# Kernel tuning notes

Hardware: AMD Instinct MI355X
Metric: run time of the kernel (lower is better)

The kernel has to match this reference:

```python
import jax, jax.numpy as jnp
import numpy as np

B, S, NGB, NG, DIM = 64, 4096, 13, 48, 3
NCH = [8, 8, 1]
NSHELLS = 8


def setup_inputs() -> dict:
    key = jax.random.key(0)
    ks = jax.random.split(key, 16)
    rng = np.random.default_rng(0)
    # valid row-wise permutations of the N_ngb neighbor slots per group op
    GnnPerms = jnp.asarray(np.argsort(rng.random((NG, NGB)), axis=1), dtype=jnp.int64)
    NNSites = jax.random.randint(ks[0], (NGB, S), 0, S, dtype=jnp.int64)
    SitesToShells = jax.random.randint(ks[1], (S,), 0, NSHELLS, dtype=jnp.int64)
    # block-diagonal (Ng*dim, Ng*dim) cartesian rotation blocks
    blk = rng.normal(size=(NG, DIM, DIM)).astype(np.float32) * 0.5
    gd = np.zeros((NG * DIM, NG * DIM), np.float32)
    for g in range(NG):
        gd[g * DIM:(g + 1) * DIM, g * DIM:(g + 1) * DIM] = blk[g]
    gdiags = jnp.asarray(gd)
    std = 0.2
    return {
        "InStates": jax.random.normal(ks[2], (B, 1, S), jnp.float32),
        "Psi0": jax.random.normal(ks[3], (NCH[0], 1, NGB), jnp.float32) * std,
        "bias0": jax.random.normal(ks[4], (NCH[0], 1), jnp.float32) * std,
        "Psi1": jax.random.normal(ks[5], (NCH[1], NCH[0], NGB), jnp.float32) * std,
        "bias1": jax.random.normal(ks[6], (NCH[1], 1), jnp.float32) * std,
        "Psi2": jax.random.normal(ks[7], (NCH[2], NCH[1], NGB), jnp.float32) * std,
        "bias2": jax.random.normal(ks[8], (NCH[2], 1), jnp.float32) * std,
        "wtVC": jax.random.normal(ks[9], (DIM, NGB), jnp.float32) * std,
        "ShellWeights": jax.random.normal(ks[10], (NSHELLS,), jnp.float32) * std,
        "gdiags": gdiags,
        "GnnPerms": GnnPerms,
        "NNSites": NNSites,
        "SitesToShells": SitesToShells,
    }


def _rearrange(x, NNSites):
    # x: (B, Nch, S) -> (B, Nch*N_ngb, S); subchannel j of channel c holds x[b, c, NNSites[j, s]]
    b, c, s = x.shape
    return x[:, :, NNSites].reshape(b, c * NGB, s)


def _gconv(x, W, b):
    # x: (B, NchIn*N_ngb, S); W: (NchOut, NchIn, N_ngb); b: (NchOut, 1)
    # group-rotated weights: GW[o, g, c*N_ngb+j] = W[o, c, GnnPerms[g, j]]
    GW = _gconv.GW_cache  # set per-call below via closure-free pattern; replaced in reference
    raise NotImplementedError


def reference(InStates, Psi0, bias0, Psi1, bias1, Psi2, bias2, wtVC,
              ShellWeights, gdiags, GnnPerms, NNSites, SitesToShells):
    act = jax.nn.softplus

    def gconv(x, W, b):
        # rotated weights: (NchOut, Ng, NchIn*N_ngb)
        GW = W[:, :, GnnPerms].transpose(0, 2, 1, 3).reshape(W.shape[0], NG, -1)
        h = jnp.einsum('ogk,bks->bogs', GW, x) + b[:, :, None]  # (B, NchOut, Ng, S)
        return act(h).mean(axis=2)                               # group-orbit average

    out = _rearrange(InStates, NNSites)
    for W, b in ((Psi0, bias0), (Psi1, bias1), (Psi2, bias2)):
        out = gconv(out, W, b)                 # (B, NchOut, S)
        out = _rearrange(out, NNSites)         # (B, NchOut*N_ngb, S)
    # vector channel: row g*dim+d of P is wtVC[d, GnnPerms[g]]
    P = wtVC[:, GnnPerms].transpose(1, 0, 2).reshape(NG * DIM, NGB)
    Wvc = gdiags @ P                           # (Ng*dim, N_ngb)
    v = jnp.einsum('kn,bns->bks', Wvc, out)    # (B, Ng*dim, S)
    v = v.reshape(-1, NG, DIM, out.shape[-1]).mean(axis=1)  # (B, dim, S)
    v = v * ShellWeights[SitesToShells]        # per-site shell weighting
    return v.sum(axis=2) / out.shape[-1]       # (B, dim)
```

## Files before the change

### kernel.cpp

```cpp
#include <hip/hip_runtime.h>
#include <hip/hip_bf16.h>

#define BATCH 64
#define SITES 4096
#define NGB 13
#define NGRP 48
#define SDIM 3

#define LOG2E 1.44269504f
#define SPSCALE 0.014440236f

typedef __bf16 bf16x8 __attribute__((ext_vector_type(8)));
typedef float  f32x4  __attribute__((ext_vector_type(4)));

#define OFF_AVC  0
#define OFF_U    64
#define OFF_A0   67648
#define OFF_SW   67648
#define OFF_A1   2164800
#define OFF_PART 4261952
#define UW0H 0
#define UW0L 12288
#define UW1H 24576
#define UW1L 73728
#define UW2H 122880
#define UW2L 129024

__global__ __launch_bounds__(256) void precompute_kernel(
    const float* __restrict__ Psi0, const float* __restrict__ Psi1,
    const float* __restrict__ Psi2, const float* __restrict__ wtVC,
    const float* __restrict__ gdiags, const int* __restrict__ perms,
    float* __restrict__ ws)
{
    float*  Avc = ws + OFF_AVC;
    __bf16* U   = (__bf16*)(ws + OFF_U);
    int t = blockIdx.x * 256 + threadIdx.x;
    if (t < 12288) {
        int k = t & 31, row = t >> 5;
        int o = row / NGRP, g = row - o * NGRP;
        float w = (k < NGB) ? Psi0[o * NGB + perms[g * NGB + k]] * LOG2E : 0.f;
        __bf16 hi = (__bf16)w;
        U[UW0H + t] = hi;
        U[UW0L + t] = (__bf16)(w - (float)hi);
    } else if (t < 61440) {
        int u = t - 12288;
        int k = u & 127, row = u >> 7;
        int o = row / NGRP, g = row - o * NGRP;
        float w = 0.f;
        if (k < 104) { int j = k >> 3, c = k & 7;
                       w = Psi1[(o * 8 + c) * NGB + perms[g * NGB + j]] * LOG2E; }
        __bf16 hi = (__bf16)w;
        U[UW1H + u] = hi;
        U[UW1L + u] = (__bf16)(w - (float)hi);
    } else if (t < 67584) {
        int u = t - 61440;
        int k = u & 127, g = u >> 7;
        float w = 0.f;
        if (k < 104) { int j = k >> 3, c = k & 7;
                       w = Psi2[c * NGB + perms[g * NGB + j]] * LOG2E; }
        __bf16 hi = (__bf16)w;
        U[UW2H + u] = hi;
        U[UW2L + u] = (__bf16)(w - (float)hi);
    } else if (t < 67584 + 39 * NGRP) {
        int t2 = t - 67584;
        int g = t2 % NGRP, u = t2 / NGRP;
        int d = u / NGB, n = u % NGB;
        const int row = g * SDIM + d;
        float s = 0.f;
        for (int k = 0; k < NGRP * SDIM; k++) {
            int g2 = k / SDIM, d2 = k - g2 * SDIM;
            float p = wtVC[d2 * NGB + perms[g2 * NGB + n]];
            s = fmaf(gdiags[row * (NGRP * SDIM) + k], p, s);
        }
        atomicAdd(&Avc[u], s * (1.f / 48.f));
    }
}

__global__ __launch_bounds__(256) void build_sw(
    const float* __restrict__ Avc, const int* __restrict__ NN,
    const int* __restrict__ s2sh, const float* __restrict__ shellw,
    float* __restrict__ SW)
{
    int e = blockIdx.x * 256 + threadIdx.x;
    if (e < NGB * SITES) {
        int n = e / SITES, s = e - n * SITES;
        float wgt = shellw[s2sh[s]] * (SPSCALE / (float)SITES);
        int t = NN[e];
        atomicAdd(&SW[t],             Avc[n] * wgt);
        atomicAdd(&SW[SITES + t],     Avc[NGB + n] * wgt);
        atomicAdd(&SW[2 * SITES + t], Avc[2 * NGB + n] * wgt);
    }
}

template<int NCIN, int NCTOT, int CT, int KPAD, int KEXT, int KSTR,
         int NWAVES, int NWN, int CHUNKS, int FUSED>
__global__ __launch_bounds__(NWAVES * 64) void layer_mfma(
    const float* __restrict__ prev,
    const __bf16* __restrict__ Wh,
    const __bf16* __restrict__ Wl,
    const float* __restrict__ bias,
    const int*   __restrict__ NN,
    const float* __restrict__ SWp,
    float* __restrict__ partial,
    float* __restrict__ out)
{
    constexpr int NTHR   = NWAVES * 64;
    constexpr int M      = NCTOT * NGRP;
    constexpr int MTILES = M / 16, NTILES = CT / 16;
    constexpr int NWM    = NWAVES / NWN;
    constexpr int MT_W   = MTILES / NWM, NT_W = NTILES / NWN;
    constexpr int KT     = KPAD / 32;
    constexpr int GS     = NGB * CT;
    constexpr int SPT    = (GS + NTHR - 1) / NTHR;
    constexpr int CPB    = SITES / CT;
    constexpr int BUF    = CT * KSTR;
    constexpr int BPB    = CPB / CHUNKS;

    static_assert(MT_W * 16 == NGRP, "wave covers exactly one o");
    static_assert(NWM * MT_W == MTILES && NWN * NT_W == NTILES, "");
    static_assert((KPAD & 31) == 0 && (KSTR & 7) == 0, "");
    static_assert(KEXT <= KPAD && (KEXT & 7) == 0 && KSTR >= KEXT, "");
    static_assert(CPB % CHUNKS == 0, "block stays within one batch");

    __shared__ __bf16 xh_lds[2 * BUF];
    __shared__ __bf16 xl_lds[2 * BUF];

    const int tid  = threadIdx.x;
    const int wave = tid >> 6, lane = tid & 63;
    const int m16  = lane & 15, quad = lane >> 4;

    const int bid    = blockIdx.x;
    const int b      = bid / BPB;
    const int octet  = bid % BPB;
    const int s0base = octet * (CHUNKS * CT);

    int sj[SPT], scol[SPT];
    bool sv[SPT];
#pragma unroll
    for (int i = 0; i < SPT; i++) {
        int site = tid + i * NTHR;
        sv[i] = (site < GS);
        int ss = sv[i] ? site : 0;
        sj[i] = ss / CT;
        scol[i] = ss % CT;
    }

    auto stage_site = [&](int i, int nn, __bf16* dh, __bf16* dl) {
        if constexpr (NCIN == 1) {
            float v = prev[(size_t)b * SITES + nn];
            __bf16 hi = (__bf16)v;
            dh[scol[i] * KSTR + sj[i]] = hi;
            dl[scol[i] * KSTR + sj[i]] = (__bf16)(v - (float)hi);
        } else {
            const float4* p4 = (const float4*)(prev + ((size_t)(b * SITES + nn)) * 8);
            float4 u0 = p4[0], u1 = p4[1];
            float v[8] = {u0.x, u0.y, u0.z, u0.w, u1.x, u1.y, u1.z, u1.w};
            bf16x8 hv, lv;
#pragma unroll
            for (int c8 = 0; c8 < 8; c8++) {
                __bf16 hi = (__bf16)v[c8];
                hv[c8] = hi;
                lv[c8] = (__bf16)(v[c8] - (float)hi);
            }
            *(bf16x8*)(dh + scol[i] * KSTR + sj[i] * 8) = hv;
            *(bf16x8*)(dl + scol[i] * KSTR + sj[i] * 8) = lv;
        }
    };

    if constexpr (NCIN == 1) {
        for (int e = tid; e < 2 * CT * (KPAD - NGB); e += NTHR) {
            int buf = e / (CT * (KPAD - NGB));
            int r   = e % (CT * (KPAD - NGB));
            int col = r / (KPAD - NGB), p = r % (KPAD - NGB);
            xh_lds[buf * BUF + col * KSTR + NGB + p] = (__bf16)0.f;
            xl_lds[buf * BUF + col * KSTR + NGB + p] = (__bf16)0.f;
        }
    }

    int nnA[SPT];
#pragma unroll
    for (int i = 0; i < SPT; i++) if (sv[i]) {
        int nn = NN[sj[i] * SITES + s0base + scol[i]];
        stage_site(i, nn, xh_lds, xl_lds);
    }
    if (CHUNKS > 1) {
        const int s1 = s0base + CT;
#pragma unroll
        for (int i = 0; i < SPT; i++)
            nnA[i] = sv[i] ? NN[sj[i] * SITES + s1 + scol[i]] : 0;
    }
    __syncthreads();

    const int wave_mt0 = (wave / NWN) * MT_W;
    const int wave_nt0 = (wave % NWN) * NT_W;
    const int o_g      = (wave_mt0 * 16) / NGRP;
    const float bo     = bias[o_g] * LOG2E;

    float y0 = 0.f, y1 = 0.f, y2 = 0.f;

#pragma unroll 1
    for (int c = 0; c < CHUNKS; c++) {
        const int cur = c & 1;
        const __bf16* xh = xh_lds + cur * BUF;
        const __bf16* xl = xl_lds + cur * BUF;

        f32x4 acc[MT_W][NT_W];
        const f32x4 binit = {bo, bo, bo, bo};
#pragma unroll
        for (int mt = 0; mt < MT_W; mt++)
#pragma unroll
            for (int nt = 0; nt < NT_W; nt++) acc[mt][nt] = binit;

#pragma unroll
        for (int kt = 0; kt < KT; kt++) {
            const int koff = kt * 32 + quad * 8;
            const int koffb = (KEXT < KPAD && koff > KEXT - 8) ? (KEXT - 8) : koff;
            bf16x8 ah[MT_W], al[MT_W], bh[NT_W], bl[NT_W];
#pragma unroll
            for (int mt = 0; mt < MT_W; mt++) {
                int row = (wave_mt0 + mt) * 16 + m16;
                ah[mt] = *(const bf16x8*)(Wh + (size_t)row * KPAD + koff);
                al[mt] = *(const bf16x8*)(Wl + (size_t)row * KPAD + koff);
            }
#pragma unroll
            for (int nt = 0; nt < NT_W; nt++) {
                int cbase = ((wave_nt0 + nt) * 16 + m16) * KSTR + koffb;
                bh[nt] = *(const bf16x8*)(xh + cbase);
                bl[nt] = *(const bf16x8*)(xl + cbase);
            }
#pragma unroll
            for (int mt = 0; mt < MT_W; mt++)
#pragma unroll
                for (int nt = 0; nt < NT_W; nt++)
                    acc[mt][nt] = __builtin_amdgcn_mfma_f32_16x16x32_bf16(
                        ah[mt], bh[nt], acc[mt][nt], 0, 0, 0);
#pragma unroll
            for (int mt = 0; mt < MT_W; mt++)
#pragma unroll
                for (int nt = 0; nt < NT_W; nt++)
                    acc[mt][nt] = __builtin_amdgcn_mfma_f32_16x16x32_bf16(
                        al[mt], bh[nt], acc[mt][nt], 0, 0, 0);
#pragma unroll
            for (int mt = 0; mt < MT_W; mt++)
#pragma unroll
                for (int nt = 0; nt < NT_W; nt++)
                    acc[mt][nt] = __builtin_amdgcn_mfma_f32_16x16x32_bf16(
                        ah[mt], bl[nt], acc[mt][nt], 0, 0, 0);
        }

        const int s0c = s0base + c * CT;
#pragma unroll
        for (int nt = 0; nt < NT_W; nt++) {
            float s = 0.f;
#pragma unroll
            for (int mt = 0; mt < MT_W; mt++)
#pragma unroll
                for (int r = 0; r < 4; r++) {
                    float h = acc[mt][nt][r];
                    s += fmaxf(h, 0.f) + __log2f(1.f + exp2f(-fabsf(h)));
                }
            s += __shfl_xor(s, 16);
            s += __shfl_xor(s, 32);
            if (quad == 0) {
                int site = s0c + (wave_nt0 + nt) * 16 + m16;
                if constexpr (FUSED) {
                    y0 = fmaf(SWp[site],             s, y0);
                    y1 = fmaf(SWp[SITES + site],     s, y1);
                    y2 = fmaf(SWp[2 * SITES + site], s, y2);
                } else {
                    out[((size_t)(b * SITES + site)) * NCTOT + o_g] = s * SPSCALE;
                }
            }
        }

        if (c + 1 < CHUNKS) {
            __bf16* dh = xh_lds + (cur ^ 1) * BUF;
            __bf16* dl = xl_lds + (cur ^ 1) * BUF;
#pragma unroll
            for (int i = 0; i < SPT; i++) if (sv[i])
                stage_site(i, nnA[i], dh, dl);
            if (c + 2 < CHUNKS) {
                const int s2 = s0base + (c + 2) * CT;
#pragma unroll
                for (int i = 0; i < SPT; i++)
                    nnA[i] = sv[i] ? NN[sj[i] * SITES + s2 + scol[i]] : 0;
            }
        }
        __syncthreads();
    }

    if constexpr (FUSED) {
        float* red = (float*)xh_lds;
        red[tid] = y0;
        red[NTHR + tid] = y1;
        red[2 * NTHR + tid] = y2;
        __syncthreads();
        for (int st = NTHR / 2; st > 0; st >>= 1) {
            if (tid < st) {
                red[tid] += red[tid + st];
                red[NTHR + tid] += red[NTHR + tid + st];
                red[2 * NTHR + tid] += red[2 * NTHR + tid + st];
            }
            __syncthreads();
        }
        if (tid < 3) partial[bid * 3 + tid] = red[tid * NTHR];
    }
}

__global__ __launch_bounds__(256) void final_sum(
    const float* __restrict__ partial, float* __restrict__ out)
{
    int t = threadIdx.x;
    if (t < BATCH * 3) {
        int b = t / 3, d = t - b * 3;
        float s = 0.f;
        for (int o = 0; o < 8; o++) s += partial[(b * 8 + o) * 3 + d];
        out[t] = s;
    }
}

extern "C" void kernel_launch(void* const* d_in, const int* in_sizes, int n_in,
                              void* d_out, int out_size, void* d_ws, size_t ws_size,
                              hipStream_t stream)
{
    const float* InStates = (const float*)d_in[0];
    const float* Psi0     = (const float*)d_in[1];
    const float* bias0    = (const float*)d_in[2];
    const float* Psi1     = (const float*)d_in[3];
    const float* bias1    = (const float*)d_in[4];
    const float* Psi2     = (const float*)d_in[5];
    const float* bias2    = (const float*)d_in[6];
    const float* wtVC     = (const float*)d_in[7];
    const float* ShellW   = (const float*)d_in[8];
    const float* gdiags   = (const float*)d_in[9];
    const int*   GnnPerms = (const int*)d_in[10];
    const int*   NNSites  = (const int*)d_in[11];
    const int*   S2Sh     = (const int*)d_in[12];

    float*  ws   = (float*)d_ws;
    float*  Avc  = ws + OFF_AVC;
    __bf16* U    = (__bf16*)(ws + OFF_U);
    float*  A0   = ws + OFF_A0;
    float*  SW   = ws + OFF_SW;
    float*  A1   = ws + OFF_A1;
    float*  PART = ws + OFF_PART;

    float* out = (float*)d_out;

    hipMemsetAsync(Avc, 0, 64 * sizeof(float), stream);
    precompute_kernel<<<272, 256, 0, stream>>>(Psi0, Psi1, Psi2, wtVC, gdiags,
                                               GnnPerms, ws);

    constexpr int CHUNKS = 8;
    constexpr int NBLK   = BATCH * (SITES / 64) / CHUNKS;

    layer_mfma<1, 8, 64, 32, 32, 40, 8, 1, CHUNKS, 0><<<NBLK, 512, 0, stream>>>(
        InStates, U + UW0H, U + UW0L, bias0, NNSites, nullptr, nullptr, A0);
    layer_mfma<8, 8, 64, 128, 104, 104, 8, 1, CHUNKS, 0><<<NBLK, 512, 0, stream>>>(
        A0, U + UW1H, U + UW1L, bias1, NNSites, nullptr, nullptr, A1);

    hipMemsetAsync(SW, 0, 3 * SITES * sizeof(float), stream);
    build_sw<<<(NGB * SITES + 255) / 256, 256, 0, stream>>>(
        Avc, NNSites, S2Sh, ShellW, SW);

    layer_mfma<8, 1, 64, 128, 104, 104, 4, 4, CHUNKS, 1><<<NBLK, 256, 0, stream>>>(
        A1, U + UW2H, U + UW2L, bias2, NNSites, SW, PART, nullptr);

    final_sum<<<1, 256, 0, stream>>>(PART, out);
}
```

Measured before the change: 310.3 us.

## Store intermediate activations pre-split as bf16 hi/lo and fold final sum into atomics

Layer outputs are now written as interleaved bf16 hi/lo pairs (16 bf16 per site) rather than fp32. The next layer can then copy the split values straight into LDS instead of reloading fp32 and converting. The final reduction kernel is removed: each block atomically adds its partial into a zeroed output buffer. This drops the per-load split arithmetic and one kernel launch, but the producer now makes scattered 2-byte stores and the atomics make the summation order nondeterministic.

After: 310.2 us. Within noise of the previous version (-0.0%).

```diff
diff --git a/kernel.cpp b/kernel.cpp
--- a/kernel.cpp
+++ b/kernel.cpp
@@ -18,7 +18,6 @@
 #define OFF_A0   67648
 #define OFF_SW   67648
 #define OFF_A1   2164800
-#define OFF_PART 4261952
 #define UW0H 0
 #define UW0L 12288
 #define UW1H 24576
@@ -95,14 +94,15 @@
 template<int NCIN, int NCTOT, int CT, int KPAD, int KEXT, int KSTR,
          int NWAVES, int NWN, int CHUNKS, int FUSED>
 __global__ __launch_bounds__(NWAVES * 64) void layer_mfma(
-    const float* __restrict__ prev,
+    const float*  __restrict__ prevF,
+    const __bf16* __restrict__ prevB,
     const __bf16* __restrict__ Wh,
     const __bf16* __restrict__ Wl,
-    const float* __restrict__ bias,
-    const int*   __restrict__ NN,
-    const float* __restrict__ SWp,
-    float* __restrict__ partial,
-    float* __restrict__ out)
+    const float*  __restrict__ bias,
+    const int*    __restrict__ NN,
+    const float*  __restrict__ SWp,
+    float* __restrict__ outAcc,
+    __bf16* __restrict__ outB)
 {
     constexpr int NTHR   = NWAVES * 64;
     constexpr int M      = NCTOT * NGRP;
@@ -147,21 +147,13 @@
 
     auto stage_site = [&](int i, int nn, __bf16* dh, __bf16* dl) {
         if constexpr (NCIN == 1) {
-            float v = prev[(size_t)b * SITES + nn];
+            float v = prevF[(size_t)b * SITES + nn];
             __bf16 hi = (__bf16)v;
             dh[scol[i] * KSTR + sj[i]] = hi;
             dl[scol[i] * KSTR + sj[i]] = (__bf16)(v - (float)hi);
         } else {
-            const float4* p4 = (const float4*)(prev + ((size_t)(b * SITES + nn)) * 8);
-            float4 u0 = p4[0], u1 = p4[1];
-            float v[8] = {u0.x, u0.y, u0.z, u0.w, u1.x, u1.y, u1.z, u1.w};
-            bf16x8 hv, lv;
-#pragma unroll
-            for (int c8 = 0; c8 < 8; c8++) {
-                __bf16 hi = (__bf16)v[c8];
-                hv[c8] = hi;
-                lv[c8] = (__bf16)(v[c8] - (float)hi);
-            }
+            const bf16x8* p = (const bf16x8*)(prevB + ((size_t)(b * SITES + nn)) * 16);
+            bf16x8 hv = p[0], lv = p[1];
             *(bf16x8*)(dh + scol[i] * KSTR + sj[i] * 8) = hv;
             *(bf16x8*)(dl + scol[i] * KSTR + sj[i] * 8) = lv;
         }
@@ -268,7 +260,11 @@
                     y1 = fmaf(SWp[SITES + site],     s, y1);
                     y2 = fmaf(SWp[2 * SITES + site], s, y2);
                 } else {
-                    out[((size_t)(b * SITES + site)) * NCTOT + o_g] = s * SPSCALE;
+                    float sv2 = s * SPSCALE;
+                    __bf16 hi = (__bf16)sv2;
+                    size_t idx = ((size_t)(b * SITES + site)) * 16;
+                    outB[idx + o_g]     = hi;
+                    outB[idx + 8 + o_g] = (__bf16)(sv2 - (float)hi);
                 }
             }
         }
@@ -303,19 +299,7 @@
             }
             __syncthreads();
         }
-        if (tid < 3) partial[bid * 3 + tid] = red[tid * NTHR];
-    }
-}
-
-__global__ __launch_bounds__(256) void final_sum(
-    const float* __restrict__ partial, float* __restrict__ out)
-{
-    int t = threadIdx.x;
-    if (t < BATCH * 3) {
-        int b = t / 3, d = t - b * 3;
-        float s = 0.f;
-        for (int o = 0; o < 8; o++) s += partial[(b * 8 + o) * 3 + d];
-        out[t] = s;
+        if (tid < 3) atomicAdd(&outAcc[b * 3 + tid], red[tid * NTHR]);
     }
 }
 
@@ -340,14 +324,14 @@
     float*  ws   = (float*)d_ws;
     float*  Avc  = ws + OFF_AVC;
     __bf16* U    = (__bf16*)(ws + OFF_U);
-    float*  A0   = ws + OFF_A0;
+    __bf16* A0   = (__bf16*)(ws + OFF_A0);
     float*  SW   = ws + OFF_SW;
-    float*  A1   = ws + OFF_A1;
-    float*  PART = ws + OFF_PART;
+    __bf16* A1   = (__bf16*)(ws + OFF_A1);
 
     float* out = (float*)d_out;
 
     hipMemsetAsync(Avc, 0, 64 * sizeof(float), stream);
+    hipMemsetAsync(out, 0, BATCH * 3 * sizeof(float), stream);
     precompute_kernel<<<272, 256, 0, stream>>>(Psi0, Psi1, Psi2, wtVC, gdiags,
                                                GnnPerms, ws);
 
@@ -355,16 +339,17 @@
     constexpr int NBLK   = BATCH * (SITES / 64) / CHUNKS;
 
     layer_mfma<1, 8, 64, 32, 32, 40, 8, 1, CHUNKS, 0><<<NBLK, 512, 0, stream>>>(
-        InStates, U + UW0H, U + UW0L, bias0, NNSites, nullptr, nullptr, A0);
+        InStates, nullptr, U + UW0H, U + UW0L, bias0, NNSites,
+        nullptr, nullptr, A0);
     layer_mfma<8, 8, 64, 128, 104, 104, 8, 1, CHUNKS, 0><<<NBLK, 512, 0, stream>>>(
-        A0, U + UW1H, U + UW1L, bias1, NNSites, nullptr, nullptr, A1);
+        nullptr, A0, U + UW1H, U + UW1L, bias1, NNSites,
+        nullptr, nullptr, A1);
 
     hipMemsetAsync(SW, 0, 3 * SITES * sizeof(float), stream);
     build_sw<<<(NGB * SITES + 255) / 256, 256, 0, stream>>>(
         Avc, NNSites, S2Sh, ShellW, SW);
 
     layer_mfma<8, 1, 64, 128, 104, 104, 4, 4, CHUNKS, 1><<<NBLK, 256, 0, stream>>>(
-        A1, U + UW2H, U + UW2L, bias2, NNSites, SW, PART, nullptr);
-
-    final_sum<<<1, 256, 0, stream>>>(PART, out);
+        nullptr, A1, U + UW2H, U + UW2L, bias2, NNSites,
+        SW, out, nullptr);
 }
```
